# Kernel optimization log

Measured on AMD Instinct MI355X. Metric: run time of the kernel, lower is better.

The kernel has to match this reference:

```python
import jax, jax.numpy as jnp
import numpy as np

T, B, F = 512, 2048, 16
H1, H2, OUT = 512, 512, 8


def gru_cell(x, h, W_ih, W_hh, b_ih, b_hh):
    # PyTorch nn.GRUCell math. W_ih: [3H, in], W_hh: [3H, H]
    gi = x @ W_ih.T + b_ih
    gh = h @ W_hh.T + b_hh
    i_r, i_z, i_n = jnp.split(gi, 3, axis=-1)
    h_r, h_z, h_n = jnp.split(gh, 3, axis=-1)
    r = jax.nn.sigmoid(i_r + h_r)
    z = jax.nn.sigmoid(i_z + h_z)
    n = jnp.tanh(i_n + r * h_n)
    return (1.0 - z) * n + z * h


def setup_inputs() -> dict:
    key = jax.random.key(0)
    ks = jax.random.split(key, 11)
    s1 = 1.0 / np.sqrt(H1)
    s2 = 1.0 / np.sqrt(H2)
    return {
        "rnn_input": jax.random.normal(ks[0], (T, B, F), dtype=jnp.float32),
        "W_ih0": jax.random.uniform(ks[1], (3 * H1, F), jnp.float32, -s1, s1),
        "W_hh0": jax.random.uniform(ks[2], (3 * H1, H1), jnp.float32, -s1, s1),
        "b_ih0": jax.random.uniform(ks[3], (3 * H1,), jnp.float32, -s1, s1),
        "b_hh0": jax.random.uniform(ks[4], (3 * H1,), jnp.float32, -s1, s1),
        "W_ih1": jax.random.uniform(ks[5], (3 * H2, H1), jnp.float32, -s2, s2),
        "W_hh1": jax.random.uniform(ks[6], (3 * H2, H2), jnp.float32, -s2, s2),
        "b_ih1": jax.random.uniform(ks[7], (3 * H2,), jnp.float32, -s2, s2),
        "b_hh1": jax.random.uniform(ks[8], (3 * H2,), jnp.float32, -s2, s2),
        "W_out": jax.random.uniform(ks[9], (OUT, H2), jnp.float32, -s2, s2),
        "b_out": jax.random.uniform(ks[10], (OUT,), jnp.float32, -s2, s2),
    }


def reference(rnn_input, W_ih0, W_hh0, b_ih0, b_hh0,
              W_ih1, W_hh1, b_ih1, b_hh1, W_out, b_out):
    batch = rnn_input.shape[1]
    h0 = jnp.zeros((batch, H1), dtype=rnn_input.dtype)
    h1 = jnp.zeros((batch, H2), dtype=rnn_input.dtype)

    def step(carry, x_t):
        h0, h1 = carry
        h0 = gru_cell(x_t, h0, W_ih0, W_hh0, b_ih0, b_hh0)
        h1 = gru_cell(h0, h1, W_ih1, W_hh1, b_ih1, b_hh1)
        return (h0, h1), None

    (h0, h1), _ = jax.lax.scan(step, (h0, h1), rnn_input)
    # forward() returns only the output at the final timestep
    return h1 @ W_out.T + b_out
```

## Files before the change

### kernel.cpp

```cpp
#include <hip/hip_runtime.h>

#define DI __device__ __forceinline__

typedef __bf16  bf16x8 __attribute__((ext_vector_type(8)));
typedef float   f32x4  __attribute__((ext_vector_type(4)));
typedef unsigned short u16;
typedef unsigned int   u32;

DI u16 f2bf(float f){ u32 u = __float_as_uint(f); u32 r = 0x7fffu + ((u>>16)&1u); return (u16)((u + r) >> 16); }
DI float bf2f(u16 h){ return __uint_as_float(((u32)h)<<16); }

union U16x8 { u16 u[8]; uint4 v; };

#define MFMA(a,b,c) __builtin_amdgcn_mfma_f32_16x16x32_bf16((a),(b),(c),0,0,0)

DI void gload16(const void* g, void* l){
  __builtin_amdgcn_global_load_lds((const __attribute__((address_space(1))) u32*)g,
                                   (__attribute__((address_space(3))) u32*)l, 16, 0, 0);
}

#define Tn 512
#define Bn 2048
#define Fn 16
#define Hn 512
#define NK32 16

#define OFF_WH0  0ull
#define OFF_WI1  3145728ull
#define OFF_WH1  6291456ull
#define OFF_WI0  9437184ull
#define OFF_H0HI 9633792ull
#define OFF_H0LO 13828096ull
#define OFF_H1HI 18022400ull
#define OFF_H1LO 22216704ull

__global__ __launch_bounds__(256) void prep_w(const float* __restrict__ w0,
                                              const float* __restrict__ w1,
                                              const float* __restrict__ w2,
                                              u16* __restrict__ dst){
  int tid = blockIdx.x*256 + threadIdx.x;
  int p = tid / 98304, rem = tid % 98304;
  int g = rem / 32768, rem2 = rem % 32768;
  int j = rem2 / 64,   k8 = rem2 % 64;
  const float* src = (p==0) ? w0 : ((p==1) ? w1 : w2);
  const float* s = src + (size_t)(g*Hn + j)*Hn + k8*8;
  U16x8 hi, lo;
#pragma unroll
  for (int i=0;i<8;++i){ float v = s[i]; u16 h = f2bf(v); hi.u[i]=h; lo.u[i]=f2bf(v - bf2f(h)); }
  size_t pairidx = (size_t)(g*32 + (j>>4))*16 + (k8>>2);
  u16* d = dst + (size_t)p*1572864 + pairidx*1024 + (size_t)((j&15) + (k8&3)*16)*8;
  *(uint4*)d = hi.v;
  *(uint4*)(d + 512) = lo.v;
}

__global__ __launch_bounds__(256) void prep_wi0(const float* __restrict__ w,
                                                u16* __restrict__ dst){
  int tid = blockIdx.x*256 + threadIdx.x;
  int g = tid / 2048, j = (tid % 2048) >> 2, k8 = tid & 3;
  U16x8 hi, lo;
  if (k8 < 2){
    const float* s = w + (size_t)(g*Hn + j)*Fn + k8*8;
#pragma unroll
    for (int i=0;i<8;++i){ float v = s[i]; u16 h = f2bf(v); hi.u[i]=h; lo.u[i]=f2bf(v - bf2f(h)); }
  } else {
#pragma unroll
    for (int i=0;i<8;++i){ hi.u[i]=0; lo.u[i]=0; }
  }
  size_t pairidx = (size_t)(g*32 + (j>>4));
  u16* d = dst + pairidx*1024 + (size_t)((j&15) + k8*16)*8;
  *(uint4*)d = hi.v;
  *(uint4*)(d + 512) = lo.v;
}

__global__ __launch_bounds__(256) void zero_ws(char* __restrict__ ws){
  int tid = blockIdx.x*256 + threadIdx.x;
  uint4 z = {0u,0u,0u,0u};
  int region = tid >> 17;
  int off = tid & 131071;
  size_t base = (region==0) ? OFF_H0HI : (region==1) ? OFF_H0LO
              : (region==2) ? OFF_H1HI : OFF_H1LO;
  *(uint4*)(ws + base + (size_t)off*16) = z;
}

template<int IS_L0>
__global__ __launch_bounds__(256, 2) void gru_step(
    const u16* __restrict__ Wi, const u16* __restrict__ Wh,
    const float* __restrict__ xsrc,
    const u16* __restrict__ Ai_hi, const u16* __restrict__ Ai_lo,
    const u16* __restrict__ Ah_hi, const u16* __restrict__ Ah_lo,
    const float* __restrict__ b_ih, const float* __restrict__ b_hh,
    u16* __restrict__ hout_hi, u16* __restrict__ hout_lo)
{
  constexpr int NI = IS_L0 ? 1 : 16;
  constexpr int NT = IS_L0 ? 17 : 32;
  __shared__ __align__(16) char smem[53248];
  const int tid  = threadIdx.x;
  const int lane = tid & 63, wv = tid >> 6;
  const int xcd = blockIdx.x & 7, idx2 = blockIdx.x >> 3;
  const int mt = idx2 >> 2, jt = xcd*4 + (idx2 & 3);

  f32x4 acc[2][4];
#pragma unroll
  for (int m=0;m<2;++m)
#pragma unroll
    for (int o=0;o<4;++o){ f32x4 z = {0.f,0.f,0.f,0.f}; acc[m][o] = z; }

  if (IS_L0){
    int b_loc = tid >> 1, kh = tid & 1;
    const float* xs = xsrc + (size_t)(mt*128 + b_loc)*Fn + kh*8;
    U16x8 u;
#pragma unroll
    for (int i=0;i<8;++i) u.u[i] = f2bf(xs[i]);
    char* dst = smem + 45056 + (b_loc>>4)*1024 + (size_t)((b_loc&15) + kh*16)*16;
    *(uint4*)dst = u.v;
    uint4 z = {0u,0u,0u,0u};
    *(uint4*)(dst + 512) = z;
  }

  auto issue = [&](int t, int bn){
    char* buf = smem + bn*22528;
    bool ish = (t >= NI);
    if (!(IS_L0 && t==0)){
      int k32 = ish ? (t - NI) : t;
      const u16* ahi = ish ? Ah_hi : Ai_hi;
      const u16* alo = ish ? Ah_lo : Ai_lo;
#pragma unroll
      for (int ii=0; ii<2; ++ii){
        int sub = ii*4 + wv;
        size_t go = ((size_t)((mt*8+sub)*NK32 + k32))*512 + (size_t)lane*8;
        gload16(ahi + go, buf +        sub*1024);
        gload16(alo + go, buf + 8192 + sub*1024);
      }
    }
    {
      const u16* w = ish ? Wh : Wi;
      int nk   = (IS_L0 && !ish) ? 1 : NK32;
      int k32w = ish ? (t - NI) : (IS_L0 ? 0 : t);
#pragma unroll
      for (int ii=0; ii<2; ++ii){
        int task = ii*4 + wv;
        if (task < 6){
          int g = task>>1, hl = task&1;
          size_t go = ((size_t)((g*32 + jt)*nk + k32w))*1024 + (size_t)hl*512 + (size_t)lane*8;
          gload16(w + go, buf + 16384 + task*1024);
        }
      }
    }
  };

  auto compute = [&](int t, int bn){
    const char* buf = smem + bn*22528;
    bf16x8 w[3][2];
#pragma unroll
    for (int g=0; g<3; ++g)
#pragma unroll
      for (int hl=0; hl<2; ++hl)
        w[g][hl] = *(const bf16x8*)(buf + 16384 + (g*2+hl)*1024 + lane*16);
    bool ish = (t >= NI);
    if (IS_L0 && t==0){
#pragma unroll
      for (int m=0;m<2;++m){
        bf16x8 ax = *(const bf16x8*)(smem + 45056 + (wv*2+m)*1024 + lane*16);
        acc[m][0] = MFMA(ax, w[0][0], acc[m][0]); acc[m][0] = MFMA(ax, w[0][1], acc[m][0]);
        acc[m][1] = MFMA(ax, w[1][0], acc[m][1]); acc[m][1] = MFMA(ax, w[1][1], acc[m][1]);
        acc[m][2] = MFMA(ax, w[2][0], acc[m][2]); acc[m][2] = MFMA(ax, w[2][1], acc[m][2]);
      }
    } else {
#pragma unroll
      for (int m=0;m<2;++m){
        bf16x8 ah = *(const bf16x8*)(buf +        (wv*2+m)*1024 + lane*16);
        bf16x8 al = *(const bf16x8*)(buf + 8192 + (wv*2+m)*1024 + lane*16);
        acc[m][0] = MFMA(ah, w[0][0], acc[m][0]);
        acc[m][0] = MFMA(ah, w[0][1], acc[m][0]);
        acc[m][0] = MFMA(al, w[0][0], acc[m][0]);
        acc[m][1] = MFMA(ah, w[1][0], acc[m][1]);
        acc[m][1] = MFMA(ah, w[1][1], acc[m][1]);
        acc[m][1] = MFMA(al, w[1][0], acc[m][1]);
        if (!ish){
          acc[m][2] = MFMA(ah, w[2][0], acc[m][2]);
          acc[m][2] = MFMA(ah, w[2][1], acc[m][2]);
          acc[m][2] = MFMA(al, w[2][0], acc[m][2]);
        } else {
          acc[m][3] = MFMA(ah, w[2][0], acc[m][3]);
          acc[m][3] = MFMA(ah, w[2][1], acc[m][3]);
          acc[m][3] = MFMA(al, w[2][0], acc[m][3]);
        }
      }
    }
  };

  issue(0, 0);
  __syncthreads();
#pragma unroll 2
  for (int t=0; t<NT; ++t){
    if (t+1 < NT) issue(t+1, (t+1)&1);
    compute(t, t&1);
    __syncthreads();
  }

  const int col = lane & 15, rg = lane >> 4;
  const int j = jt*16 + col;
  const float bir = b_ih[j], biz = b_ih[Hn + j], bin = b_ih[2*Hn + j];
  const float bhr = b_hh[j], bhz = b_hh[Hn + j], bhn = b_hh[2*Hn + j];
#pragma unroll
  for (int m=0;m<2;++m){
    int brow = mt*128 + wv*32 + m*16 + rg*4;
#pragma unroll
    for (int r=0;r<4;++r){
      int b = brow + r;
      float pr  = acc[m][0][r] + bir + bhr;
      float pz  = acc[m][1][r] + biz + bhz;
      float pin = acc[m][2][r] + bin;
      float phn = acc[m][3][r] + bhn;
      float rgt = 1.f/(1.f + __expf(-pr));
      float zgt = 1.f/(1.f + __expf(-pz));
      float e2  = __expf(2.f*(pin + rgt*phn));
      float nn  = 1.f - 2.f/(e2 + 1.f);
      size_t fo = ((size_t)(b>>4)*NK32 + (j>>5))*512 + (size_t)((b&15) + ((j>>3)&3)*16)*8 + (j&7);
      float hv  = bf2f(Ah_hi[fo]) + bf2f(Ah_lo[fo]);
      float hnv = (1.f - zgt)*nn + zgt*hv;
      u16 hi = f2bf(hnv);
      u16 lo = f2bf(hnv - bf2f(hi));
      hout_hi[fo] = hi; hout_lo[fo] = lo;
    }
  }
}

__global__ __launch_bounds__(64) void outproj(const u16* __restrict__ h1hi,
                                              const u16* __restrict__ h1lo,
                                              const float* __restrict__ Wout,
                                              const float* __restrict__ bout,
                                              float* __restrict__ out){
  int b = blockIdx.x, l = threadIdx.x;
  float a[8] = {0.f,0.f,0.f,0.f,0.f,0.f,0.f,0.f};
  for (int jj = l; jj < Hn; jj += 64){
    size_t fo = ((size_t)(b>>4)*NK32 + (jj>>5))*512 + (size_t)((b&15) + ((jj>>3)&3)*16)*8 + (jj&7);
    float hv = bf2f(h1hi[fo]) + bf2f(h1lo[fo]);
#pragma unroll
    for (int o=0;o<8;++o) a[o] += hv * Wout[o*Hn + jj];
  }
#pragma unroll
  for (int o=0;o<8;++o){
#pragma unroll
    for (int off=32; off; off>>=1) a[o] += __shfl_xor(a[o], off);
  }
  if (l == 0){
#pragma unroll
    for (int o=0;o<8;++o) out[b*8+o] = a[o] + bout[o];
  }
}

extern "C" void kernel_launch(void* const* d_in, const int* in_sizes, int n_in,
                              void* d_out, int out_size, void* d_ws, size_t ws_size,
                              hipStream_t stream){
  (void)in_sizes; (void)n_in; (void)out_size; (void)ws_size;
  const float* x    = (const float*)d_in[0];
  const float* Wih0 = (const float*)d_in[1];
  const float* Whh0 = (const float*)d_in[2];
  const float* bih0 = (const float*)d_in[3];
  const float* bhh0 = (const float*)d_in[4];
  const float* Wih1 = (const float*)d_in[5];
  const float* Whh1 = (const float*)d_in[6];
  const float* bih1 = (const float*)d_in[7];
  const float* bhh1 = (const float*)d_in[8];
  const float* Wout = (const float*)d_in[9];
  const float* bout = (const float*)d_in[10];
  char* ws = (char*)d_ws;

  u16* WH0 = (u16*)(ws + OFF_WH0);
  const u16* WI1 = (const u16*)(ws + OFF_WI1);
  const u16* WH1 = (const u16*)(ws + OFF_WH1);
  const u16* WI0 = (const u16*)(ws + OFF_WI0);
  u16 *H0HI = (u16*)(ws + OFF_H0HI), *H0LO = (u16*)(ws + OFF_H0LO);
  u16 *H1HI = (u16*)(ws + OFF_H1HI), *H1LO = (u16*)(ws + OFF_H1LO);

  prep_w  <<<1152, 256, 0, stream>>>(Whh0, Wih1, Whh1, WH0);
  prep_wi0<<<  24, 256, 0, stream>>>(Wih0, (u16*)(ws + OFF_WI0));
  zero_ws <<<2048, 256, 0, stream>>>(ws);

  for (int s = 0; s < Tn; ++s){
    int rp = s & 1, wp = rp ^ 1;
    gru_step<1><<<512, 256, 0, stream>>>(
        WI0, (const u16*)WH0,
        x + (size_t)s*Bn*Fn,
        nullptr, nullptr,
        H0HI + (size_t)rp*1048576, H0LO + (size_t)rp*1048576,
        bih0, bhh0,
        H0HI + (size_t)wp*1048576, H0LO + (size_t)wp*1048576);
    gru_step<0><<<512, 256, 0, stream>>>(
        WI1, WH1,
        nullptr,
        H0HI + (size_t)wp*1048576, H0LO + (size_t)wp*1048576,
        H1HI + (size_t)rp*1048576, H1LO + (size_t)rp*1048576,
        bih1, bhh1,
        H1HI + (size_t)wp*1048576, H1LO + (size_t)wp*1048576);
  }

  outproj<<<2048, 64, 0, stream>>>(
      H1HI, H1LO, Wout, bout, (float*)d_out);
}
```

Baseline: 21.19 ms.

## Load activations into registers and deepen weight pipeline with manual vmcnt waits

```diff
diff --git a/kernel.cpp b/kernel.cpp
--- a/kernel.cpp
+++ b/kernel.cpp
@@ -11,12 +11,27 @@
 DI float bf2f(u16 h){ return __uint_as_float(((u32)h)<<16); }
 
 union U16x8 { u16 u[8]; uint4 v; };
+union AB    { uint4 u; bf16x8 b; };
 
 #define MFMA(a,b,c) __builtin_amdgcn_mfma_f32_16x16x32_bf16((a),(b),(c),0,0,0)
 
 DI void gload16(const void* g, void* l){
   __builtin_amdgcn_global_load_lds((const __attribute__((address_space(1))) u32*)g,
                                    (__attribute__((address_space(3))) u32*)l, 16, 0, 0);
+}
+DI void aload(uint4& d, const void* p){
+  asm volatile("global_load_dwordx4 %0, %1, off" : "=&v"(d) : "v"(p) : "memory");
+}
+template<int N> DI void wait_vmcnt(){ asm volatile("s_waitcnt vmcnt(%0)" :: "n"(N) : "memory"); }
+DI void vwait(int n){
+  switch(n){
+    case 0:  wait_vmcnt<0>();  break;
+    case 4:  wait_vmcnt<4>();  break;
+    case 8:  wait_vmcnt<8>();  break;
+    case 9:  wait_vmcnt<9>();  break;
+    case 10: wait_vmcnt<10>(); break;
+    default: wait_vmcnt<12>(); break;
+  }
 }
 
 #define Tn 512
@@ -93,11 +108,12 @@
 {
   constexpr int NI = IS_L0 ? 1 : 16;
   constexpr int NT = IS_L0 ? 17 : 32;
-  __shared__ __align__(16) char smem[53248];
+  __shared__ __align__(16) char smem[45056];
   const int tid  = threadIdx.x;
   const int lane = tid & 63, wv = tid >> 6;
-  const int xcd = blockIdx.x & 7, idx2 = blockIdx.x >> 3;
-  const int mt = idx2 >> 2, jt = xcd*4 + (idx2 & 3);
+  const int bid = blockIdx.x;
+  const int mt = (bid & 7)*2 + ((bid >> 3) & 1);
+  const int jt = bid >> 4;
 
   f32x4 acc[2][4];
 #pragma unroll
@@ -111,56 +127,56 @@
     U16x8 u;
 #pragma unroll
     for (int i=0;i<8;++i) u.u[i] = f2bf(xs[i]);
-    char* dst = smem + 45056 + (b_loc>>4)*1024 + (size_t)((b_loc&15) + kh*16)*16;
+    char* dst = smem + 36864 + (b_loc>>4)*1024 + (size_t)((b_loc&15) + kh*16)*16;
     *(uint4*)dst = u.v;
     uint4 z = {0u,0u,0u,0u};
     *(uint4*)(dst + 512) = z;
   }
 
-  auto issue = [&](int t, int bn){
-    char* buf = smem + bn*22528;
-    bool ish = (t >= NI);
-    if (!(IS_L0 && t==0)){
-      int k32 = ish ? (t - NI) : t;
-      const u16* ahi = ish ? Ah_hi : Ai_hi;
-      const u16* alo = ish ? Ah_lo : Ai_lo;
-#pragma unroll
-      for (int ii=0; ii<2; ++ii){
-        int sub = ii*4 + wv;
-        size_t go = ((size_t)((mt*8+sub)*NK32 + k32))*512 + (size_t)lane*8;
-        gload16(ahi + go, buf +        sub*1024);
-        gload16(alo + go, buf + 8192 + sub*1024);
-      }
-    }
-    {
-      const u16* w = ish ? Wh : Wi;
-      int nk   = (IS_L0 && !ish) ? 1 : NK32;
-      int k32w = ish ? (t - NI) : (IS_L0 ? 0 : t);
-#pragma unroll
-      for (int ii=0; ii<2; ++ii){
-        int task = ii*4 + wv;
-        if (task < 6){
-          int g = task>>1, hl = task&1;
-          size_t go = ((size_t)((g*32 + jt)*nk + k32w))*1024 + (size_t)hl*512 + (size_t)lane*8;
-          gload16(w + go, buf + 16384 + task*1024);
-        }
-      }
+  uint4 areg[16];
+
+  auto issueW = [&](int s){
+    char* buf = smem + (s % 6)*6144;
+    bool ish = (s >= NI);
+    const u16* w; int nk, k32w;
+    if (IS_L0 && !ish){ w = Wi; nk = 1; k32w = 0; }
+    else { w = ish ? Wh : Wi; nk = NK32; k32w = ish ? (s - NI) : s; }
+    int ntask = (wv < 2) ? 2 : 1;
+    int tbase = (wv < 2) ? wv*2 : (2 + wv);
+    for (int ii=0; ii<ntask; ++ii){
+      int task = tbase + ii, g = task >> 1, hl = task & 1;
+      size_t go = ((size_t)((g*32 + jt)*nk + k32w))*1024 + (size_t)hl*512 + (size_t)lane*8;
+      gload16(w + go, buf + task*1024);
     }
   };
 
-  auto compute = [&](int t, int bn){
-    const char* buf = smem + bn*22528;
+  auto issueA = [&](int s, uint4* dst){
+    bool ish = (s >= NI);
+    if (IS_L0 && !ish) return;
+    int k32 = ish ? (s - NI) : s;
+    const u16* ahi = ish ? Ah_hi : Ai_hi;
+    const u16* alo = ish ? Ah_lo : Ai_lo;
+#pragma unroll
+    for (int m=0;m<2;++m){
+      size_t go = ((size_t)((mt*8 + wv*2 + m)*NK32 + k32))*512 + (size_t)lane*8;
+      aload(dst[m*2],   ahi + go);
+      aload(dst[m*2+1], alo + go);
+    }
+  };
+
+  auto compute = [&](int t, const uint4* ar){
+    const char* buf = smem + (t % 6)*6144;
     bf16x8 w[3][2];
 #pragma unroll
     for (int g=0; g<3; ++g)
 #pragma unroll
       for (int hl=0; hl<2; ++hl)
-        w[g][hl] = *(const bf16x8*)(buf + 16384 + (g*2+hl)*1024 + lane*16);
+        w[g][hl] = *(const bf16x8*)(buf + (g*2+hl)*1024 + lane*16);
     bool ish = (t >= NI);
     if (IS_L0 && t==0){
 #pragma unroll
       for (int m=0;m<2;++m){
-        bf16x8 ax = *(const bf16x8*)(smem + 45056 + (wv*2+m)*1024 + lane*16);
+        bf16x8 ax = *(const bf16x8*)(smem + 36864 + (wv*2+m)*1024 + lane*16);
         acc[m][0] = MFMA(ax, w[0][0], acc[m][0]); acc[m][0] = MFMA(ax, w[0][1], acc[m][0]);
         acc[m][1] = MFMA(ax, w[1][0], acc[m][1]); acc[m][1] = MFMA(ax, w[1][1], acc[m][1]);
         acc[m][2] = MFMA(ax, w[2][0], acc[m][2]); acc[m][2] = MFMA(ax, w[2][1], acc[m][2]);
@@ -168,8 +184,8 @@
     } else {
 #pragma unroll
       for (int m=0;m<2;++m){
-        bf16x8 ah = *(const bf16x8*)(buf +        (wv*2+m)*1024 + lane*16);
-        bf16x8 al = *(const bf16x8*)(buf + 8192 + (wv*2+m)*1024 + lane*16);
+        AB cah, cal; cah.u = ar[m*2]; cal.u = ar[m*2+1];
+        bf16x8 ah = cah.b, al = cal.b;
         acc[m][0] = MFMA(ah, w[0][0], acc[m][0]);
         acc[m][0] = MFMA(ah, w[0][1], acc[m][0]);
         acc[m][0] = MFMA(al, w[0][0], acc[m][0]);
@@ -189,13 +205,27 @@
     }
   };
 
-  issue(0, 0);
-  __syncthreads();
-#pragma unroll 2
+  issueW(0); issueW(1); issueW(2); issueW(3); issueW(4);
+  issueA(0, &areg[0]); issueA(1, &areg[4]); issueA(2, &areg[8]);
+  asm volatile("s_waitcnt lgkmcnt(0)" ::: "memory");
+
+#pragma unroll
   for (int t=0; t<NT; ++t){
-    if (t+1 < NT) issue(t+1, (t+1)&1);
-    compute(t, t&1);
-    __syncthreads();
+    int d = NT-1-t;
+    int lv01, lv23;
+    if      (t==0){ lv01=8;  lv23=8; }
+    else if (t==1){ lv01=10; lv23=9; }
+    else if (d>=4){ lv01=12; lv23=10; }
+    else if (d==3){ lv01=10; lv23=9; }
+    else if (d==2){ lv01=8;  lv23=8; }
+    else if (d==1){ lv01=4;  lv23=4; }
+    else          { lv01=0;  lv23=0; }
+    if (wv < 2) vwait(lv01); else vwait(lv23);
+    __builtin_amdgcn_sched_barrier(0);
+    __builtin_amdgcn_s_barrier();
+    compute(t, &areg[(t&3)*4]);
+    if (t+5 < NT) issueW(t+5);
+    if (t+3 < NT) issueA(t+3, &areg[((t+3)&3)*4]);
   }
 
   const int col = lane & 15, rg = lane >> 4;
```

Result: faster. 17.92 ms (-15.4%).
